# Optimization experiments

Measured on AMD Instinct MI355X. Metric: run time of the kernel, lower is better.

Reference implementation:

```python
import jax, jax.numpy as jnp
import numpy as np

D = 1024      # mapped_dim
M = 5         # num_ref_modes
H = 112
W = 112


def setup_inputs() -> dict:
    key = jax.random.key(0)
    ks = jax.random.split(key, 9)
    roi_signal = jax.random.randint(ks[0], (1, 1, H, W), 0, M, dtype=jnp.int32)
    roi_features = jax.random.normal(ks[1], (1, D, H, W), dtype=jnp.float32)
    roi_mask = jax.random.uniform(ks[2], (1, 1, H, W), dtype=jnp.float32)
    s = np.float32(1.0 / np.sqrt(D))
    patch_embed = jax.random.normal(ks[3], (M, D), dtype=jnp.float32) * np.float32(np.sqrt(2.0 / (M + D)))
    Wq = jax.random.normal(ks[4], (D, D), dtype=jnp.float32) * s
    Wk = jax.random.normal(ks[5], (D, D), dtype=jnp.float32) * s
    Wv = jax.random.normal(ks[6], (D, D), dtype=jnp.float32) * s
    bq = jnp.zeros((D,), jnp.float32)
    bk = jnp.zeros((D,), jnp.float32)
    bv = jnp.zeros((D,), jnp.float32)
    conv_w = jax.random.normal(ks[7], (1, D), dtype=jnp.float32) * s  # 1x1 conv, out=1
    conv_b = jnp.zeros((1,), jnp.float32)
    return dict(roi_signal=roi_signal, roi_features=roi_features, roi_mask=roi_mask,
                patch_embed=patch_embed, Wq=Wq, bq=bq, Wk=Wk, bk=bk, Wv=Wv, bv=bv,
                conv_w=conv_w, conv_b=conv_b)


def reference(roi_signal, roi_features, roi_mask, patch_embed, Wq, bq, Wk, bk, Wv, bv, conv_w, conv_b):
    _, _, ROI_H, ROI_W = roi_mask.shape
    d = roi_features.shape[1]
    # ref_embed: one_hot(ref_label) @ patch_embed == gather; (1,1,H,W) -> (1,H,W,D) -> (1,D,H,W)
    pe = jnp.transpose(patch_embed[roi_signal[:, 0]], (0, 3, 1, 2))
    xA = roi_features + pe
    # flatten to tokens: (D, N).T -> (N, D)
    A = xA.reshape(d, -1).T
    O = roi_features.reshape(d, -1).T
    Q = A @ Wq.T + bq
    K = O @ Wk.T + bk
    V = O @ Wv.T + bv
    scores = (Q @ K.T) / jnp.sqrt(jnp.float32(d))        # (N, N) -- dominant intermediate
    attn = jax.nn.softmax(scores, axis=-1)
    out = attn @ V                                        # (N, D)
    # 1x1 conv classification head == per-token dot with conv_w
    seg = (out @ conv_w.T + conv_b).reshape(1, 1, ROI_H, ROI_W)
    return jax.nn.sigmoid(seg.astype(jnp.float32))
```

## Files before the change

### kernel.cpp

```cpp
#include <hip/hip_runtime.h>
#include <math.h>


#define DD 1024
#define NN 12544
#define NSPLIT 5
#define NPART  10
#define NTILES 49

typedef __attribute__((ext_vector_type(8))) short short8;
typedef __attribute__((ext_vector_type(4))) float f32x4;
typedef __attribute__((ext_vector_type(4))) unsigned short ushort4_t;
typedef unsigned short ushort_t;
typedef unsigned int uint32;

__device__ __forceinline__ ushort_t f2bf(float f) {
    union { float f; uint32 u; } v; v.f = f;
    uint32 u = v.u + 0x7FFF + ((v.u >> 16) & 1);
    return (ushort_t)(u >> 16);
}

__device__ __forceinline__ void gload_lds16(const void* g, void* l) {
    __builtin_amdgcn_global_load_lds((const __attribute__((address_space(1))) uint32*)g,
                                     (__attribute__((address_space(3))) uint32*)l, 16, 0, 0);
}

__global__ void k_u(const float* __restrict__ Wv, const float* __restrict__ cw,
                    const float* __restrict__ bv, float* __restrict__ u,
                    float* __restrict__ cptr) {
    const int t = threadIdx.x;
    const int k = blockIdx.x * 256 + t;
    const int d0 = blockIdx.y * 64;
    float acc = 0.f;
#pragma unroll 16
    for (int i = 0; i < 64; ++i) acc += Wv[(size_t)(d0 + i) * DD + k] * cw[d0 + i];
    atomicAdd(&u[k], acc);
    if (blockIdx.x == 0 && t < 64) {
        float ca = bv[d0 + t] * cw[d0 + t];
        for (int off = 32; off > 0; off >>= 1) ca += __shfl_down(ca, off);
        if (t == 0) atomicAdd(cptr, ca);
    }
}

__global__ __launch_bounds__(256)
void k_prep(const float* __restrict__ rf, const int* __restrict__ sig,
            const float* __restrict__ pe, const float* __restrict__ u,
            ushort_t* __restrict__ xo, ushort_t* __restrict__ xa,
            float* __restrict__ vsc) {
    __shared__ ushort_t so[64][136];
    __shared__ ushort_t sa[64][136];
    __shared__ float pel[5 * 128];
    __shared__ float ul[128];
    __shared__ int sigl[64];
    __shared__ f32x4 red[16][16];
    const int t = threadIdx.x;
    const int n0 = blockIdx.x * 64;
    if (t < 64) sigl[t] = sig[n0 + t];
    __syncthreads();
    const int dl = t >> 4, tg = t & 15;
    const int sg[4] = {sigl[tg * 4], sigl[tg * 4 + 1], sigl[tg * 4 + 2], sigl[tg * 4 + 3]};
    const int tok = t >> 2, part = t & 3;
    f32x4 vacc = (f32x4)(0.f);

    for (int c = 0; c < 8; ++c) {
        const int d0 = c * 128;
        for (int i = t; i < 640; i += 256) pel[i] = pe[(i >> 7) * DD + d0 + (i & 127)];
        if (t < 128) ul[t] = u[d0 + t];
        __syncthreads();
#pragma unroll
        for (int s = 0; s < 8; ++s) {
            const int dli = s * 16 + dl;
            const f32x4 x = *(const f32x4*)&rf[(size_t)(d0 + dli) * NN + n0 + tg * 4];
            vacc += x * ul[dli];
            ushort_t oo[4], aa[4];
#pragma unroll
            for (int j = 0; j < 4; ++j) {
                oo[j] = f2bf(x[j]);
                aa[j] = f2bf(x[j] + pel[sg[j] * 128 + dli]);
            }
#pragma unroll
            for (int j = 0; j < 4; ++j) {
                so[tg * 4 + j][dli] = oo[j];
                sa[tg * 4 + j][dli] = aa[j];
            }
        }
        __syncthreads();
#pragma unroll
        for (int i = 0; i < 4; ++i) {
            const int off = part * 32 + i * 8;
            *(short8*)&xo[(size_t)(n0 + tok) * DD + d0 + off] = *(const short8*)&so[tok][off];
            *(short8*)&xa[(size_t)(n0 + tok) * DD + d0 + off] = *(const short8*)&sa[tok][off];
        }
        __syncthreads();
    }
    red[dl][tg] = vacc;
    __syncthreads();
    if (t < 64) {
        float s = 0.f;
#pragma unroll
        for (int i = 0; i < 16; ++i) s += ((const float*)&red[i][t >> 2])[t & 3];
        vsc[n0 + t] = s;
    }
}

__global__ void k_wcast(const float* __restrict__ Wq, const float* __restrict__ Wk,
                        ushort_t* __restrict__ wqb, ushort_t* __restrict__ wkb) {
    const int idx = (blockIdx.x * 256 + threadIdx.x) * 8;
    const float* src = blockIdx.y ? Wk : Wq;
    ushort_t* dst = blockIdx.y ? wkb : wqb;
    f32x4 a = *(const f32x4*)&src[idx];
    f32x4 b = *(const f32x4*)&src[idx + 4];
    short8 o;
#pragma unroll
    for (int j = 0; j < 4; ++j) { o[j] = (short)f2bf(a[j]); o[4 + j] = (short)f2bf(b[j]); }
    *(short8*)&dst[idx] = o;
}

__global__ __launch_bounds__(256, 2)
void k_pgemm(const ushort_t* __restrict__ xb, const ushort_t* __restrict__ wb,
             const float* __restrict__ bias, float scale, ushort_t* __restrict__ outb) {
    __shared__ ushort_t as_[128 * 64];
    __shared__ ushort_t bs_[128 * 64];
    const int t = threadIdx.x;
    const int wv = t >> 6, ln = t & 63;
    const int wr = wv >> 1, wc = wv & 1;
    const int l15 = ln & 15, lhi = ln >> 4;
    const int n0 = blockIdx.x * 128;
    const int m0 = blockIdx.y * 128;
    const int srow = wv * 32;
    const int lr = ln >> 3, lc = ln & 7;
    const int swz = lc ^ lr;

    f32x4 acc[4][4];
#pragma unroll
    for (int a = 0; a < 4; ++a)
#pragma unroll
        for (int b = 0; b < 4; ++b) acc[a][b] = (f32x4)(0.f);

    for (int kk = 0; kk < DD; kk += 64) {
        __syncthreads();
#pragma unroll
        for (int i = 0; i < 4; ++i) {
            const int tok = srow + i * 8 + lr;
            gload_lds16(wb + (size_t)(m0 + tok) * DD + kk + (swz << 3), as_ + (srow + i * 8) * 64);
            gload_lds16(xb + (size_t)(n0 + tok) * DD + kk + (swz << 3), bs_ + (srow + i * 8) * 64);
        }
        __syncthreads();
#pragma unroll
        for (int kp = 0; kp < 2; ++kp) {
            short8 af[4], bf_[4];
#pragma unroll
            for (int mi = 0; mi < 4; ++mi) {
                int r = wr * 64 + mi * 16 + l15;
                int cch = (kp * 4 + lhi) ^ (r & 7);
                af[mi] = *(const short8*)(as_ + r * 64 + cch * 8);
            }
#pragma unroll
            for (int ni = 0; ni < 4; ++ni) {
                int r = wc * 64 + ni * 16 + l15;
                int cch = (kp * 4 + lhi) ^ (r & 7);
                bf_[ni] = *(const short8*)(bs_ + r * 64 + cch * 8);
            }
#pragma unroll
            for (int mi = 0; mi < 4; ++mi)
#pragma unroll
                for (int ni = 0; ni < 4; ++ni)
                    acc[mi][ni] = __builtin_amdgcn_mfma_f32_16x16x32_bf16(
                        af[mi], bf_[ni], acc[mi][ni], 0, 0, 0);
        }
    }
    float bb[4][4];
#pragma unroll
    for (int mi = 0; mi < 4; ++mi) {
        f32x4 b4 = *(const f32x4*)&bias[m0 + wr * 64 + mi * 16 + lhi * 4];
#pragma unroll
        for (int r = 0; r < 4; ++r) bb[mi][r] = b4[r];
    }
#pragma unroll
    for (int mi = 0; mi < 4; ++mi)
#pragma unroll
        for (int ni = 0; ni < 4; ++ni) {
            ushort4_t o;
#pragma unroll
            for (int r = 0; r < 4; ++r) o[r] = f2bf((acc[mi][ni][r] + bb[mi][r]) * scale);
            *(ushort4_t*)&outb[(size_t)(n0 + wc * 64 + ni * 16 + l15) * DD +
                               m0 + wr * 64 + mi * 16 + lhi * 4] = o;
        }
}

__global__ __launch_bounds__(512, 2)
void k_attn(const ushort_t* __restrict__ qb, const ushort_t* __restrict__ kb,
            const float* __restrict__ vsc, float* __restrict__ pm,
            float* __restrict__ pl, float* __restrict__ pa) {
    __shared__ ushort_t As[2][256 * 32];
    __shared__ ushort_t Bs[2][256 * 32];
    const int t = threadIdx.x;
    const int wv = t >> 6, ln = t & 63;
    const int wm = wv >> 1, wn = wv & 1;
    const int l15 = ln & 15, lhi = ln >> 4;

    const int g = blockIdx.x;
    const int xcd = g & 7, gq = g >> 3;
    const int L = (xcd < 5) ? xcd * 31 + gq : 155 + (xcd - 5) * 30 + gq;
    const int bx = L / NSPLIT, split = L % NSPLIT;
    const int m0 = bx * 256;

    const int srow0 = (ln >> 2);
    const int spc = ln & 3;

    float rm[4][4], rl[4][4], ra[4][4];
#pragma unroll
    for (int a = 0; a < 4; ++a)
#pragma unroll
        for (int b = 0; b < 4; ++b) { rm[a][b] = -INFINITY; rl[a][b] = 0.f; ra[a][b] = 0.f; }

    f32x4 acc[4][8];
#pragma unroll
    for (int a = 0; a < 4; ++a)
#pragma unroll
        for (int b = 0; b < 8; ++b) acc[a][b] = (f32x4)(0.f);

    int cur = 0;
    {
        const int n0 = split * 256;
#pragma unroll
        for (int s2 = 0; s2 < 2; ++s2) {
            const int seg = wv * 2 + s2;
            const int row = seg * 16 + srow0;
            const int c = spc ^ ((row >> 1) & 3);
            gload_lds16(qb + (size_t)(m0 + row) * DD + c * 8, &As[0][seg * 512]);
            gload_lds16(kb + (size_t)(n0 + row) * DD + c * 8, &Bs[0][seg * 512]);
        }
    }
    __syncthreads();

    for (int nt = split; nt < NTILES; nt += NSPLIT) {
        const int n0 = nt * 256;
        for (int kidx = 0; kidx < 32; ++kidx) {
            int nk = kidx + 1, nnt = nt;
            if (nk == 32) { nk = 0; nnt = nt + NSPLIT; }
            if (nnt < NTILES) {
                const int nn0 = nnt * 256;
                const int kko = nk * 32;
                ushort_t* Ad = &As[cur ^ 1][0];
                ushort_t* Bd = &Bs[cur ^ 1][0];
#pragma unroll
                for (int s2 = 0; s2 < 2; ++s2) {
                    const int seg = wv * 2 + s2;
                    const int row = seg * 16 + srow0;
                    const int c = spc ^ ((row >> 1) & 3);
                    gload_lds16(qb + (size_t)(m0 + row) * DD + kko + c * 8, Ad + seg * 512);
                    gload_lds16(kb + (size_t)(nn0 + row) * DD + kko + c * 8, Bd + seg * 512);
                }
            }
            const ushort_t* Ab = &As[cur][0];
            const ushort_t* Bb = &Bs[cur][0];
            short8 af[4], bfr[8];
#pragma unroll
            for (int mi = 0; mi < 4; ++mi) {
                const int row = wm * 64 + mi * 16 + l15;
                const int phys = lhi ^ ((row >> 1) & 3);
                af[mi] = *(const short8*)(Ab + row * 32 + phys * 8);
            }
#pragma unroll
            for (int ni = 0; ni < 8; ++ni) {
                const int row = wn * 128 + ni * 16 + l15;
                const int phys = lhi ^ ((row >> 1) & 3);
                bfr[ni] = *(const short8*)(Bb + row * 32 + phys * 8);
            }
            __builtin_amdgcn_s_setprio(1);
#pragma unroll
            for (int ni = 0; ni < 8; ++ni)
#pragma unroll
                for (int mi = 0; mi < 4; ++mi)
                    acc[mi][ni] = __builtin_amdgcn_mfma_f32_16x16x32_bf16(
                        af[mi], bfr[ni], acc[mi][ni], 0, 0, 0);
            __builtin_amdgcn_s_setprio(0);
            __syncthreads();
            cur ^= 1;
        }
        float vv[8];
#pragma unroll
        for (int ni = 0; ni < 8; ++ni) vv[ni] = vsc[n0 + wn * 128 + ni * 16 + l15];
#pragma unroll
        for (int mi = 0; mi < 4; ++mi) {
#pragma unroll
            for (int r = 0; r < 4; ++r) {
                float mx = acc[mi][0][r];
#pragma unroll
                for (int ni = 1; ni < 8; ++ni) mx = fmaxf(mx, acc[mi][ni][r]);
                mx = fmaxf(mx, __shfl_xor(mx, 1));
                mx = fmaxf(mx, __shfl_xor(mx, 2));
                mx = fmaxf(mx, __shfl_xor(mx, 4));
                mx = fmaxf(mx, __shfl_xor(mx, 8));
                const float mnew = fmaxf(rm[mi][r], mx);
                float sp = 0.f, sv = 0.f;
#pragma unroll
                for (int ni = 0; ni < 8; ++ni) {
                    float p = __expf(acc[mi][ni][r] - mnew);
                    sp += p; sv += p * vv[ni];
                }
                sp += __shfl_xor(sp, 1); sv += __shfl_xor(sv, 1);
                sp += __shfl_xor(sp, 2); sv += __shfl_xor(sv, 2);
                sp += __shfl_xor(sp, 4); sv += __shfl_xor(sv, 4);
                sp += __shfl_xor(sp, 8); sv += __shfl_xor(sv, 8);
                const float f = __expf(rm[mi][r] - mnew);
                rl[mi][r] = rl[mi][r] * f + sp;
                ra[mi][r] = ra[mi][r] * f + sv;
                rm[mi][r] = mnew;
            }
        }
#pragma unroll
        for (int a = 0; a < 4; ++a)
#pragma unroll
            for (int b = 0; b < 8; ++b) acc[a][b] = (f32x4)(0.f);
    }
    if (l15 == 0) {
        const size_t slab = (size_t)(split * 2 + wn) * NN;
#pragma unroll
        for (int mi = 0; mi < 4; ++mi)
#pragma unroll
            for (int r = 0; r < 4; ++r) {
                int row = m0 + wm * 64 + mi * 16 + lhi * 4 + r;
                pm[slab + row] = rm[mi][r];
                pl[slab + row] = rl[mi][r];
                pa[slab + row] = ra[mi][r];
            }
    }
}

__global__ void k_comb(const float* __restrict__ pm, const float* __restrict__ pl,
                       const float* __restrict__ pa, const float* __restrict__ cptr,
                       const float* __restrict__ cb, float* __restrict__ out) {
    int n = blockIdx.x * 256 + threadIdx.x;
    float gm = -INFINITY;
#pragma unroll
    for (int s = 0; s < NPART; ++s) gm = fmaxf(gm, pm[(size_t)s * NN + n]);
    float l = 0.f, a = 0.f;
#pragma unroll
    for (int s = 0; s < NPART; ++s) {
        float f = __expf(pm[(size_t)s * NN + n] - gm);
        l += pl[(size_t)s * NN + n] * f;
        a += pa[(size_t)s * NN + n] * f;
    }
    float x = a / l + cptr[0] + cb[0];
    out[n] = 1.f / (1.f + __expf(-x));
}

extern "C" void kernel_launch(void* const* d_in, const int* in_sizes, int n_in,
                              void* d_out, int out_size, void* d_ws, size_t ws_size,
                              hipStream_t stream) {
    const int* sig = (const int*)d_in[0];
    const float* rf = (const float*)d_in[1];
    const float* pe = (const float*)d_in[3];
    const float* Wq = (const float*)d_in[4];
    const float* bq = (const float*)d_in[5];
    const float* Wk = (const float*)d_in[6];
    const float* bk = (const float*)d_in[7];
    const float* Wv = (const float*)d_in[8];
    const float* bv = (const float*)d_in[9];
    const float* cw = (const float*)d_in[10];
    const float* cb = (const float*)d_in[11];
    float* out = (float*)d_out;

    ushort_t* buf0 = (ushort_t*)d_ws;
    ushort_t* buf1 = buf0 + (size_t)NN * DD;
    ushort_t* buf2 = buf1 + (size_t)NN * DD;
    ushort_t* wqb = buf2 + (size_t)NN * DD;
    ushort_t* wkb = wqb + (size_t)DD * DD;
    float* u = (float*)(wkb + (size_t)DD * DD);
    float* cptr = u + 1024;
    float* vsc = u + 1024 + 16;
    float* pm = vsc + NN;
    float* pl = pm + (size_t)NPART * NN;
    float* pa = pl + (size_t)NPART * NN;

    hipMemsetAsync(u, 0, (1024 + 16) * sizeof(float), stream);
    k_u<<<dim3(4, 16), 256, 0, stream>>>(Wv, cw, bv, u, cptr);
    k_prep<<<196, 256, 0, stream>>>(rf, sig, pe, u, buf0, buf1, vsc);
    k_wcast<<<dim3(512, 2), 256, 0, stream>>>(Wq, Wk, wqb, wkb);
    k_pgemm<<<dim3(98, 8), 256, 0, stream>>>(buf0, wkb, bk, 1.0f, buf2);
    k_pgemm<<<dim3(98, 8), 256, 0, stream>>>(buf1, wqb, bq, 0.03125f, buf0);
    k_attn<<<245, 512, 0, stream>>>(buf0, buf2, vsc, pm, pl, pa);
    k_comb<<<NN / 256, 256, 0, stream>>>(pm, pl, pa, cptr, cb, out);
}
```

Before: 541.5 us.

## Double K-step per barrier in attention kernel with XOR-8 swizzled LDS and fused softmax

The attention QK^T main loop now stages 64-wide K slices instead of 32, so each barrier covers two MFMA sub-steps and the number of barriers and global-to-LDS load rounds per tile is halved. The LDS layout changes to 64-element rows with an XOR-8 swizzle to keep bank conflicts low. The online-softmax update is moved inside the last K iteration, before the barrier, so it overlaps with the prefetch of the next tile. The cost is LDS use doubling to 128 KB per block, which at launch bounds (512,2) may limit occupancy to one block per CU.

Result: faster. 484.3 us (-10.6%).

```diff
diff --git a/kernel.cpp b/kernel.cpp
--- a/kernel.cpp
+++ b/kernel.cpp
@@ -192,8 +192,8 @@
 void k_attn(const ushort_t* __restrict__ qb, const ushort_t* __restrict__ kb,
             const float* __restrict__ vsc, float* __restrict__ pm,
             float* __restrict__ pl, float* __restrict__ pa) {
-    __shared__ ushort_t As[2][256 * 32];
-    __shared__ ushort_t Bs[2][256 * 32];
+    __shared__ ushort_t As[2][256 * 64];
+    __shared__ ushort_t Bs[2][256 * 64];
     const int t = threadIdx.x;
     const int wv = t >> 6, ln = t & 63;
     const int wm = wv >> 1, wn = wv & 1;
@@ -205,8 +205,8 @@
     const int bx = L / NSPLIT, split = L % NSPLIT;
     const int m0 = bx * 256;
 
-    const int srow0 = (ln >> 2);
-    const int spc = ln & 3;
+    const int srw = (ln >> 3);
+    const int sch = ln & 7;
 
     float rm[4][4], rl[4][4], ra[4][4];
 #pragma unroll
@@ -224,96 +224,101 @@
     {
         const int n0 = split * 256;
 #pragma unroll
-        for (int s2 = 0; s2 < 2; ++s2) {
-            const int seg = wv * 2 + s2;
-            const int row = seg * 16 + srow0;
-            const int c = spc ^ ((row >> 1) & 3);
-            gload_lds16(qb + (size_t)(m0 + row) * DD + c * 8, &As[0][seg * 512]);
-            gload_lds16(kb + (size_t)(n0 + row) * DD + c * 8, &Bs[0][seg * 512]);
-        }
-    }
-    __syncthreads();
+        for (int b = 0; b < 4; ++b) {
+            const int r = b * 64 + wv * 8 + srw;
+            const int soff = (sch ^ (r & 7)) << 3;
+            gload_lds16(qb + (size_t)(m0 + r) * DD + soff, &As[0][(b * 64 + wv * 8) * 64]);
+            gload_lds16(kb + (size_t)(n0 + r) * DD + soff, &Bs[0][(b * 64 + wv * 8) * 64]);
+        }
+    }
+    asm volatile("s_waitcnt vmcnt(0)" ::: "memory");
+    __builtin_amdgcn_s_barrier();
 
     for (int nt = split; nt < NTILES; nt += NSPLIT) {
         const int n0 = nt * 256;
-        for (int kidx = 0; kidx < 32; ++kidx) {
+        for (int kidx = 0; kidx < 16; ++kidx) {
             int nk = kidx + 1, nnt = nt;
-            if (nk == 32) { nk = 0; nnt = nt + NSPLIT; }
+            if (nk == 16) { nk = 0; nnt = nt + NSPLIT; }
             if (nnt < NTILES) {
+                const int kko = nk * 64;
                 const int nn0 = nnt * 256;
-                const int kko = nk * 32;
                 ushort_t* Ad = &As[cur ^ 1][0];
                 ushort_t* Bd = &Bs[cur ^ 1][0];
 #pragma unroll
-                for (int s2 = 0; s2 < 2; ++s2) {
-                    const int seg = wv * 2 + s2;
-                    const int row = seg * 16 + srow0;
-                    const int c = spc ^ ((row >> 1) & 3);
-                    gload_lds16(qb + (size_t)(m0 + row) * DD + kko + c * 8, Ad + seg * 512);
-                    gload_lds16(kb + (size_t)(nn0 + row) * DD + kko + c * 8, Bd + seg * 512);
+                for (int b = 0; b < 4; ++b) {
+                    const int r = b * 64 + wv * 8 + srw;
+                    const int soff = kko + ((sch ^ (r & 7)) << 3);
+                    gload_lds16(qb + (size_t)(m0 + r) * DD + soff, Ad + (b * 64 + wv * 8) * 64);
+                    gload_lds16(kb + (size_t)(nn0 + r) * DD + soff, Bd + (b * 64 + wv * 8) * 64);
                 }
             }
             const ushort_t* Ab = &As[cur][0];
             const ushort_t* Bb = &Bs[cur][0];
-            short8 af[4], bfr[8];
-#pragma unroll
-            for (int mi = 0; mi < 4; ++mi) {
-                const int row = wm * 64 + mi * 16 + l15;
-                const int phys = lhi ^ ((row >> 1) & 3);
-                af[mi] = *(const short8*)(Ab + row * 32 + phys * 8);
-            }
-#pragma unroll
-            for (int ni = 0; ni < 8; ++ni) {
-                const int row = wn * 128 + ni * 16 + l15;
-                const int phys = lhi ^ ((row >> 1) & 3);
-                bfr[ni] = *(const short8*)(Bb + row * 32 + phys * 8);
-            }
-            __builtin_amdgcn_s_setprio(1);
-#pragma unroll
-            for (int ni = 0; ni < 8; ++ni)
-#pragma unroll
-                for (int mi = 0; mi < 4; ++mi)
-                    acc[mi][ni] = __builtin_amdgcn_mfma_f32_16x16x32_bf16(
-                        af[mi], bfr[ni], acc[mi][ni], 0, 0, 0);
-            __builtin_amdgcn_s_setprio(0);
-            __syncthreads();
+#pragma unroll
+            for (int kp = 0; kp < 2; ++kp) {
+                short8 af[4], bfr[8];
+#pragma unroll
+                for (int mi = 0; mi < 4; ++mi) {
+                    const int r = wm * 64 + mi * 16 + l15;
+                    const int c = (kp * 4 + lhi) ^ (r & 7);
+                    af[mi] = *(const short8*)(Ab + r * 64 + c * 8);
+                }
+#pragma unroll
+                for (int ni = 0; ni < 8; ++ni) {
+                    const int r = wn * 128 + ni * 16 + l15;
+                    const int c = (kp * 4 + lhi) ^ (r & 7);
+                    bfr[ni] = *(const short8*)(Bb + r * 64 + c * 8);
+                }
+                __builtin_amdgcn_s_setprio(1);
+#pragma unroll
+                for (int ni = 0; ni < 8; ++ni)
+#pragma unroll
+                    for (int mi = 0; mi < 4; ++mi)
+                        acc[mi][ni] = __builtin_amdgcn_mfma_f32_16x16x32_bf16(
+                            af[mi], bfr[ni], acc[mi][ni], 0, 0, 0);
+                __builtin_amdgcn_s_setprio(0);
+            }
+            if (kidx == 15) {
+                float vv[8];
+#pragma unroll
+                for (int ni = 0; ni < 8; ++ni) vv[ni] = vsc[n0 + wn * 128 + ni * 16 + l15];
+#pragma unroll
+                for (int mi = 0; mi < 4; ++mi) {
+#pragma unroll
+                    for (int r = 0; r < 4; ++r) {
+                        float mx = acc[mi][0][r];
+#pragma unroll
+                        for (int ni = 1; ni < 8; ++ni) mx = fmaxf(mx, acc[mi][ni][r]);
+                        mx = fmaxf(mx, __shfl_xor(mx, 1));
+                        mx = fmaxf(mx, __shfl_xor(mx, 2));
+                        mx = fmaxf(mx, __shfl_xor(mx, 4));
+                        mx = fmaxf(mx, __shfl_xor(mx, 8));
+                        const float mnew = fmaxf(rm[mi][r], mx);
+                        float sp = 0.f, sv = 0.f;
+#pragma unroll
+                        for (int ni = 0; ni < 8; ++ni) {
+                            float p = __expf(acc[mi][ni][r] - mnew);
+                            sp += p; sv += p * vv[ni];
+                        }
+                        sp += __shfl_xor(sp, 1); sv += __shfl_xor(sv, 1);
+                        sp += __shfl_xor(sp, 2); sv += __shfl_xor(sv, 2);
+                        sp += __shfl_xor(sp, 4); sv += __shfl_xor(sv, 4);
+                        sp += __shfl_xor(sp, 8); sv += __shfl_xor(sv, 8);
+                        const float f = __expf(rm[mi][r] - mnew);
+                        rl[mi][r] = rl[mi][r] * f + sp;
+                        ra[mi][r] = ra[mi][r] * f + sv;
+                        rm[mi][r] = mnew;
+                    }
+                }
+#pragma unroll
+                for (int a = 0; a < 4; ++a)
+#pragma unroll
+                    for (int b = 0; b < 8; ++b) acc[a][b] = (f32x4)(0.f);
+            }
+            asm volatile("s_waitcnt vmcnt(0)" ::: "memory");
+            __builtin_amdgcn_s_barrier();
             cur ^= 1;
         }
-        float vv[8];
-#pragma unroll
-        for (int ni = 0; ni < 8; ++ni) vv[ni] = vsc[n0 + wn * 128 + ni * 16 + l15];
-#pragma unroll
-        for (int mi = 0; mi < 4; ++mi) {
-#pragma unroll
-            for (int r = 0; r < 4; ++r) {
-                float mx = acc[mi][0][r];
-#pragma unroll
-                for (int ni = 1; ni < 8; ++ni) mx = fmaxf(mx, acc[mi][ni][r]);
-                mx = fmaxf(mx, __shfl_xor(mx, 1));
-                mx = fmaxf(mx, __shfl_xor(mx, 2));
-                mx = fmaxf(mx, __shfl_xor(mx, 4));
-                mx = fmaxf(mx, __shfl_xor(mx, 8));
-                const float mnew = fmaxf(rm[mi][r], mx);
-                float sp = 0.f, sv = 0.f;
-#pragma unroll
-                for (int ni = 0; ni < 8; ++ni) {
-                    float p = __expf(acc[mi][ni][r] - mnew);
-                    sp += p; sv += p * vv[ni];
-                }
-                sp += __shfl_xor(sp, 1); sv += __shfl_xor(sv, 1);
-                sp += __shfl_xor(sp, 2); sv += __shfl_xor(sv, 2);
-                sp += __shfl_xor(sp, 4); sv += __shfl_xor(sv, 4);
-                sp += __shfl_xor(sp, 8); sv += __shfl_xor(sv, 8);
-                const float f = __expf(rm[mi][r] - mnew);
-                rl[mi][r] = rl[mi][r] * f + sp;
-                ra[mi][r] = ra[mi][r] * f + sv;
-                rm[mi][r] = mnew;
-            }
-        }
-#pragma unroll
-        for (int a = 0; a < 4; ++a)
-#pragma unroll
-            for (int b = 0; b < 8; ++b) acc[a][b] = (f32x4)(0.f);
     }
     if (l15 == 0) {
         const size_t slab = (size_t)(split * 2 + wn) * NN;
```
